# Performance work log

Hardware: AMD Instinct MI355X
Metric: run time of the kernel (lower is better)

## Reference

```python
import jax, jax.numpy as jnp
import numpy as np

B, S, T = 64, 48, 48
E, H = 256, 512
VIN, VOUT = 32000, 32000


def _gru_step(h, x, Wih, Whh, bih, bhh):
    # PyTorch GRU cell: gates ordered [r, z, n]
    gi = x @ Wih.T + bih            # [B, 3H]
    gh = h @ Whh.T + bhh            # [B, 3H]
    ir, iz, inn = jnp.split(gi, 3, axis=-1)
    hr, hz, hn = jnp.split(gh, 3, axis=-1)
    r = jax.nn.sigmoid(ir + hr)
    z = jax.nn.sigmoid(iz + hz)
    n = jnp.tanh(inn + r * hn)
    return (1.0 - z) * n + z * h


def setup_inputs() -> dict:
    key = jax.random.key(0)
    ks = jax.random.split(key, 24)
    scale = 0.05

    def w(k, shape):
        return jax.random.normal(k, shape, dtype=jnp.float32) * scale

    return {
        "source": jax.random.randint(ks[0], (B, S), 0, VIN),
        "target": jax.random.randint(ks[1], (B, T), 0, VOUT),
        "source_lengths": jax.random.randint(ks[2], (B,), 1, S + 1),
        "enc_emb": w(ks[3], (VIN, E)),
        "enc_Wih0": w(ks[4], (3 * H, E)),
        "enc_Whh0": w(ks[5], (3 * H, H)),
        "enc_bih0": w(ks[6], (3 * H,)),
        "enc_bhh0": w(ks[7], (3 * H,)),
        "enc_Wih1": w(ks[8], (3 * H, H)),
        "enc_Whh1": w(ks[9], (3 * H, H)),
        "enc_bih1": w(ks[10], (3 * H,)),
        "enc_bhh1": w(ks[11], (3 * H,)),
        "dec_emb": w(ks[12], (VOUT, E)),
        "dec_Wih0": w(ks[13], (3 * H, E)),
        "dec_Whh0": w(ks[14], (3 * H, H)),
        "dec_bih0": w(ks[15], (3 * H,)),
        "dec_bhh0": w(ks[16], (3 * H,)),
        "dec_Wih1": w(ks[17], (3 * H, H)),
        "dec_Whh1": w(ks[18], (3 * H, H)),
        "dec_bih1": w(ks[19], (3 * H,)),
        "dec_bhh1": w(ks[20], (3 * H,)),
        "fc_W": w(ks[21], (VOUT, H)),
        "fc_b": w(ks[22], (VOUT,)),
    }


def reference(source, target, source_lengths,
              enc_emb, enc_Wih0, enc_Whh0, enc_bih0, enc_bhh0,
              enc_Wih1, enc_Whh1, enc_bih1, enc_bhh1,
              dec_emb, dec_Wih0, dec_Whh0, dec_bih0, dec_bhh0,
              dec_Wih1, dec_Whh1, dec_bih1, dec_bhh1,
              fc_W, fc_b):
    # ---- Encoder: 2-layer GRU over packed (length-masked) source ----
    emb = enc_emb[source]                       # [B, S, E]
    xs = jnp.transpose(emb, (1, 0, 2))          # [S, B, E]
    ts = jnp.arange(S)
    h0 = jnp.zeros((B, H), emb.dtype)
    h1 = jnp.zeros((B, H), emb.dtype)

    def estep(carry, inp):
        c0, c1 = carry
        x_t, t = inp
        m = (t < source_lengths)[:, None]       # valid-step mask (packing semantics)
        n0 = _gru_step(c0, x_t, enc_Wih0, enc_Whh0, enc_bih0, enc_bhh0)
        n1 = _gru_step(c1, n0, enc_Wih1, enc_Whh1, enc_bih1, enc_bhh1)
        return (jnp.where(m, n0, c0), jnp.where(m, n1, c1)), None

    (h0, h1), _ = jax.lax.scan(estep, (h0, h1), (xs, ts))

    # ---- Decoder: teacher forcing (ratio=1.0) -> inputs are target[:, :-1] ----
    dec_in = dec_emb[target[:, :-1]]            # [B, T-1, E]
    dxs = jnp.transpose(dec_in, (1, 0, 2))      # [T-1, B, E]

    def dstep(carry, x_t):
        c0, c1 = carry
        n0 = _gru_step(c0, x_t, dec_Wih0, dec_Whh0, dec_bih0, dec_bhh0)
        n1 = _gru_step(c1, n0, dec_Wih1, dec_Whh1, dec_bih1, dec_bhh1)
        return (n0, n1), n1

    _, ys = jax.lax.scan(dstep, (h0, h1), dxs)  # [T-1, B, H]
    logits = jnp.einsum('tbh,vh->btv', ys, fc_W) + fc_b  # [B, T-1, V]
    # outputs[:, 0, :] stays zero as in the torch loop (starts at t=1)
    return jnp.concatenate([jnp.zeros((B, 1, VOUT), logits.dtype), logits], axis=1)
```

## Files before the change

kernel.cpp:

```cpp
#include <hip/hip_runtime.h>

#define B_    64
#define S_    48
#define T_    48
#define E_    256
#define H_    512
#define G_    1536
#define VOUT_ 32000
#define NBLK_ 48

typedef __attribute__((ext_vector_type(8))) short short8;
typedef __attribute__((ext_vector_type(4))) float f4;

__device__ inline unsigned short f2bf(float f) {
    unsigned u = __float_as_uint(f);
    u += 0x7fffu + ((u >> 16) & 1u);
    return (unsigned short)(u >> 16);
}
__device__ inline unsigned pack2(float a, float b) {
    return (unsigned)f2bf(a) | ((unsigned)f2bf(b) << 16);
}

__global__ void zero_f32(float* p, int n) {
    int i = blockIdx.x * 256 + threadIdx.x;
    if (i < n) p[i] = 0.f;
}

__global__ void zero_out_t0(float* out) {
    int v = blockIdx.x * 256 + threadIdx.x;
    int b = blockIdx.y;
    if (v < VOUT_) out[(size_t)b * T_ * VOUT_ + v] = 0.f;
}

__global__ void cvt_bf16(const float* __restrict__ s, unsigned short* __restrict__ d, int n4) {
    int i = blockIdx.x * 256 + threadIdx.x;
    if (i < n4) {
        float4 v = ((const float4*)s)[i];
        uint2 o;
        o.x = pack2(v.x, v.y);
        o.y = pack2(v.z, v.w);
        ((uint2*)d)[i] = o;
    }
}

__global__ __launch_bounds__(256)
void gemm64(const float* __restrict__ aF,
            const unsigned short* __restrict__ aB,
            const int* __restrict__ idx, int idx_stride,
            const unsigned short* __restrict__ Wb,
            const float* __restrict__ bias,
            float* __restrict__ outF,
            float* __restrict__ outR,
            int N, int K)
{
    __shared__ __align__(16) short As[64][40];
    __shared__ __align__(16) short Ws[64][40];
    const int tid  = threadIdx.x;
    const int m0   = blockIdx.x * 64;
    const int n0   = blockIdx.y * 64;
    const int row  = tid >> 2;
    const int col8 = (tid & 3) * 8;

    const float* apF = nullptr;
    const unsigned short* apB = nullptr;
    {
        int m = m0 + row;
        if (aF) {
            size_t r;
            if (idx) { int tt = m >> 6, b = m & 63; r = (size_t)idx[b * idx_stride + tt]; }
            else     { r = (size_t)m; }
            apF = aF + r * K + col8;
        } else {
            apB = aB + (size_t)m * K + col8;
        }
    }
    const unsigned short* wp = Wb + (size_t)(n0 + row) * K + col8;

    f4 acc[4];
    const f4 zz = {0.f, 0.f, 0.f, 0.f};
    acc[0] = zz; acc[1] = zz; acc[2] = zz; acc[3] = zz;

    const int wv   = tid >> 6;
    const int lane = tid & 63;
    const int quad = lane >> 4;
    const int l16  = lane & 15;

    for (int k0 = 0; k0 < K; k0 += 32) {
        uint4 av;
        if (apF) {
            float4 v0 = *(const float4*)(apF + k0);
            float4 v1 = *(const float4*)(apF + k0 + 4);
            av.x = pack2(v0.x, v0.y);
            av.y = pack2(v0.z, v0.w);
            av.z = pack2(v1.x, v1.y);
            av.w = pack2(v1.z, v1.w);
        } else {
            av = *(const uint4*)(apB + k0);
        }
        uint4 wvv = *(const uint4*)(wp + k0);
        *(uint4*)&As[row][col8] = av;
        *(uint4*)&Ws[row][col8] = wvv;
        __syncthreads();
        short8 afrag = *(const short8*)&As[wv * 16 + l16][quad * 8];
#pragma unroll
        for (int nt = 0; nt < 4; ++nt) {
            short8 bfrag = *(const short8*)&Ws[nt * 16 + l16][quad * 8];
            acc[nt] = __builtin_amdgcn_mfma_f32_16x16x32_bf16(afrag, bfrag, acc[nt], 0, 0, 0);
        }
        __syncthreads();
    }

#pragma unroll
    for (int nt = 0; nt < 4; ++nt) {
#pragma unroll
        for (int r = 0; r < 4; ++r) {
            int mm = m0 + wv * 16 + quad * 4 + r;
            int nn = n0 + nt * 16 + l16;
            float v = acc[nt][r];
            if (bias) v += bias[nn];
            if (outF) {
                outF[(size_t)mm * N + nn] = v;
            } else {
                int tt = mm >> 6, b = mm & 63;
                outR[((size_t)b * T_ + tt + 1) * VOUT_ + nn] = v;
            }
        }
    }
}

__device__ __forceinline__ void gsync(unsigned* bar, unsigned target) {
    __syncthreads();
    if (threadIdx.x == 0) {
        __threadfence();
        __hip_atomic_fetch_add(bar, 1u, __ATOMIC_RELAXED, __HIP_MEMORY_SCOPE_AGENT);
        while (__hip_atomic_load(bar, __ATOMIC_RELAXED, __HIP_MEMORY_SCOPE_AGENT) < target) {
            __builtin_amdgcn_s_sleep(1);
        }
        __threadfence();
    }
    __syncthreads();
}

__global__ __launch_bounds__(256, 1)
void scan_rnn(const unsigned short* __restrict__ Whh0,
              const unsigned short* __restrict__ Wih1,
              const unsigned short* __restrict__ Whh1,
              const float* __restrict__ gi,
              const float* __restrict__ bih1,
              const float* __restrict__ bhh0,
              const float* __restrict__ bhh1,
              float* __restrict__ h0F, float* __restrict__ h1F,
              unsigned short* __restrict__ h0b0, unsigned short* __restrict__ h0b1,
              unsigned short* __restrict__ h1b0, unsigned short* __restrict__ h1b1,
              unsigned short* __restrict__ n0b0, unsigned short* __restrict__ n0b1,
              unsigned short* __restrict__ ys,
              const int* __restrict__ lens,
              unsigned* __restrict__ bar, unsigned bar_base, int nsteps)
{
    __shared__ __align__(16) short8 Wl[96][64];

    const int tid   = threadIdx.x;
    const int bid   = blockIdx.x;
    const int wv    = tid >> 6;
    const int lane  = tid & 63;
    const int quad  = lane >> 4;
    const int l16   = lane & 15;
    const int quad8 = quad * 8;
    const int rowA  = wv * 16 + l16;
    const int mrow  = wv * 16 + quad * 4;
    const bool isL0 = bid < 16;
    const int j0    = isL0 ? bid * 32 : (bid - 16) * 16;
    const f4 zz = {0.f, 0.f, 0.f, 0.f};

#pragma unroll 4
    for (int i = 0; i < 24; ++i) {
        const int f = wv * 24 + i;
        const unsigned short* src;
        if (isL0) {
            int kiter = f / 6, rem = f % 6, g = rem >> 1, nt = rem & 1;
            src = Whh0 + (size_t)(g * H_ + j0 + nt * 16 + l16) * H_ + kiter * 32 + quad8;
        } else {
            int p = f / 48, rem = f % 48, kiter = rem / 3, g = rem % 3;
            const unsigned short* W = p ? Whh1 : Wih1;
            src = W + (size_t)(g * H_ + j0 + l16) * H_ + kiter * 32 + quad8;
        }
        Wl[f][lane] = *(const short8*)src;
    }
    __syncthreads();

    int lenm[4];
#pragma unroll
    for (int r = 0; r < 4; ++r) lenm[r] = lens ? lens[mrow + r] : 0x7fffffff;

    float b0r[2], b0z[2], b0n[2], h0r[2][4];
    float b1r = 0.f, b1z = 0.f, b1in = 0.f, b1hn = 0.f, h1r[4];
    if (isL0) {
#pragma unroll
        for (int nt = 0; nt < 2; ++nt) {
            const int j = j0 + nt * 16 + l16;
            b0r[nt] = bhh0[j]; b0z[nt] = bhh0[j + H_]; b0n[nt] = bhh0[j + 2 * H_];
#pragma unroll
            for (int r = 0; r < 4; ++r) h0r[nt][r] = h0F[(mrow + r) * H_ + j];
        }
    } else {
        const int j = j0 + l16;
        b1r  = bhh1[j] + bih1[j];
        b1z  = bhh1[j + H_] + bih1[j + H_];
        b1in = bih1[j + 2 * H_];
        b1hn = bhh1[j + 2 * H_];
#pragma unroll
        for (int r = 0; r < 4; ++r) h1r[r] = h1F[(mrow + r) * H_ + j];
    }

    for (int s = 0; s <= nsteps; ++s) {
        float gir[2][4], giz[2][4], gin[2][4];
        if (isL0 && s < nsteps) {
            const float* giT = gi + (size_t)s * (B_ * G_);
#pragma unroll
            for (int nt = 0; nt < 2; ++nt) {
                const int j = j0 + nt * 16 + l16;
#pragma unroll
                for (int r = 0; r < 4; ++r) {
                    const float* g = giT + (size_t)(mrow + r) * G_;
                    gir[nt][r] = g[j];
                    giz[nt][r] = g[j + H_];
                    gin[nt][r] = g[j + 2 * H_];
                }
            }
        }
        if (s) gsync(bar, bar_base + (unsigned)(NBLK_ * s));

        if (isL0) {
            const int t = s;
            if (t >= nsteps) continue;
            const int pi = t & 1;
            const unsigned short* Ab = pi ? h0b1 : h0b0;
            unsigned short* hob = pi ? h0b0 : h0b1;
            unsigned short* nob = pi ? n0b1 : n0b0;

            short8 av[16];
#pragma unroll
            for (int k = 0; k < 16; ++k)
                av[k] = *(const short8*)(Ab + (size_t)rowA * H_ + k * 32 + quad8);

            f4 acc[4][2];
#pragma unroll
            for (int a = 0; a < 4; ++a) { acc[a][0] = zz; acc[a][1] = zz; }
#pragma unroll
            for (int k = 0; k < 16; ++k) {
#pragma unroll
                for (int g = 0; g < 3; ++g) {
                    const int ai = (g == 2) ? 3 : g;
#pragma unroll
                    for (int nt = 0; nt < 2; ++nt) {
                        acc[ai][nt] = __builtin_amdgcn_mfma_f32_16x16x32_bf16(
                            av[k], Wl[k * 6 + g * 2 + nt][lane], acc[ai][nt], 0, 0, 0);
                    }
                }
            }

#pragma unroll
            for (int nt = 0; nt < 2; ++nt) {
                const int j = j0 + nt * 16 + l16;
#pragma unroll
                for (int r = 0; r < 4; ++r) {
                    const int m = mrow + r;
                    float pr = acc[0][nt][r] + b0r[nt] + gir[nt][r];
                    float pz = acc[1][nt][r] + b0z[nt] + giz[nt][r];
                    float hn = acc[3][nt][r] + b0n[nt];
                    float rg = 1.f / (1.f + expf(-pr));
                    float zg = 1.f / (1.f + expf(-pz));
                    float ng = tanhf(gin[nt][r] + rg * hn);
                    float hp = h0r[nt][r];
                    float hnew = (1.f - zg) * ng + zg * hp;
                    nob[m * H_ + j] = f2bf(hnew);
                    float hw = (t >= lenm[r]) ? hp : hnew;
                    h0r[nt][r] = hw;
                    hob[m * H_ + j] = f2bf(hw);
                    if (t == nsteps - 1) h0F[m * H_ + j] = hw;
                }
            }
        } else {
            const int t = s - 1;
            if (t < 0) continue;
            const int pi = t & 1;
            const unsigned short* xb = pi ? n0b1 : n0b0;
            const unsigned short* hb = pi ? h1b1 : h1b0;
            unsigned short* hob = pi ? h1b0 : h1b1;

            short8 av0[16], av1[16];
#pragma unroll
            for (int k = 0; k < 16; ++k) {
                av0[k] = *(const short8*)(xb + (size_t)rowA * H_ + k * 32 + quad8);
                av1[k] = *(const short8*)(hb + (size_t)rowA * H_ + k * 32 + quad8);
            }

            f4 acc[4];
#pragma unroll
            for (int a = 0; a < 4; ++a) acc[a] = zz;
#pragma unroll
            for (int k = 0; k < 16; ++k) {
#pragma unroll
                for (int g = 0; g < 3; ++g) {
                    const int ai = (g == 2) ? 2 : g;
                    acc[ai] = __builtin_amdgcn_mfma_f32_16x16x32_bf16(
                        av0[k], Wl[k * 3 + g][lane], acc[ai], 0, 0, 0);
                }
            }
#pragma unroll
            for (int k = 0; k < 16; ++k) {
#pragma unroll
                for (int g = 0; g < 3; ++g) {
                    const int ai = (g == 2) ? 3 : g;
                    acc[ai] = __builtin_amdgcn_mfma_f32_16x16x32_bf16(
                        av1[k], Wl[48 + k * 3 + g][lane], acc[ai], 0, 0, 0);
                }
            }

            const int j = j0 + l16;
#pragma unroll
            for (int r = 0; r < 4; ++r) {
                const int m = mrow + r;
                float pr  = acc[0][r] + b1r;
                float pz  = acc[1][r] + b1z;
                float inn = acc[2][r] + b1in;
                float hn  = acc[3][r] + b1hn;
                float rg = 1.f / (1.f + expf(-pr));
                float zg = 1.f / (1.f + expf(-pz));
                float ng = tanhf(inn + rg * hn);
                float hp = h1r[r];
                float hnew = (1.f - zg) * ng + zg * hp;
                if (ys) ys[((size_t)t * B_ + m) * H_ + j] = f2bf(hnew);
                float hw = (t >= lenm[r]) ? hp : hnew;
                h1r[r] = hw;
                hob[m * H_ + j] = f2bf(hw);
                if (t == nsteps - 1) h1F[m * H_ + j] = hw;
            }
        }
    }
}

static inline void cvt(const float* s, unsigned short* d, int n, hipStream_t st) {
    int n4 = n / 4;
    cvt_bf16<<<dim3((n4 + 255) / 256), 256, 0, st>>>(s, d, n4);
}

extern "C" void kernel_launch(void* const* d_in, const int* in_sizes, int n_in,
                              void* d_out, int out_size, void* d_ws, size_t ws_size,
                              hipStream_t stream)
{
    const int* source  = (const int*)d_in[0];
    const int* target  = (const int*)d_in[1];
    const int* src_len = (const int*)d_in[2];
    const float* enc_emb  = (const float*)d_in[3];
    const float* enc_Wih0 = (const float*)d_in[4];
    const float* enc_Whh0 = (const float*)d_in[5];
    const float* enc_bih0 = (const float*)d_in[6];
    const float* enc_bhh0 = (const float*)d_in[7];
    const float* enc_Wih1 = (const float*)d_in[8];
    const float* enc_Whh1 = (const float*)d_in[9];
    const float* enc_bih1 = (const float*)d_in[10];
    const float* enc_bhh1 = (const float*)d_in[11];
    const float* dec_emb  = (const float*)d_in[12];
    const float* dec_Wih0 = (const float*)d_in[13];
    const float* dec_Whh0 = (const float*)d_in[14];
    const float* dec_bih0 = (const float*)d_in[15];
    const float* dec_bhh0 = (const float*)d_in[16];
    const float* dec_Wih1 = (const float*)d_in[17];
    const float* dec_Whh1 = (const float*)d_in[18];
    const float* dec_bih1 = (const float*)d_in[19];
    const float* dec_bhh1 = (const float*)d_in[20];
    const float* fc_W     = (const float*)d_in[21];
    const float* fc_b     = (const float*)d_in[22];
    float* out = (float*)d_out;

    const size_t BH = (size_t)B_ * H_;

    char* w = (char*)d_ws;
    float* h0F = (float*)w;           w += BH * 4;
    float* h1F = (float*)w;           w += BH * 4;
    unsigned short* h0b0 = (unsigned short*)w; w += BH * 2;
    unsigned short* h1b0 = (unsigned short*)w; w += BH * 2;
    unsigned* bar = (unsigned*)w;     w += 256;
    unsigned short* h0b1 = (unsigned short*)w; w += BH * 2;
    unsigned short* h1b1 = (unsigned short*)w; w += BH * 2;
    unsigned short* n0b0 = (unsigned short*)w; w += BH * 2;
    unsigned short* n0b1 = (unsigned short*)w; w += BH * 2;
    float* gi_buf = (float*)w;                w += (size_t)S_ * B_ * G_ * 4;
    unsigned short* ys = (unsigned short*)w;  w += (size_t)(T_ - 1) * B_ * H_ * 2;
    unsigned short* eWih0b = (unsigned short*)w; w += (size_t)G_ * E_ * 2;
    unsigned short* dWih0b = (unsigned short*)w; w += (size_t)G_ * E_ * 2;
    unsigned short* eWih1b = (unsigned short*)w; w += (size_t)G_ * H_ * 2;
    unsigned short* eWhh0b = (unsigned short*)w; w += (size_t)G_ * H_ * 2;
    unsigned short* eWhh1b = (unsigned short*)w; w += (size_t)G_ * H_ * 2;
    unsigned short* dWih1b = (unsigned short*)w; w += (size_t)G_ * H_ * 2;
    unsigned short* dWhh0b = (unsigned short*)w; w += (size_t)G_ * H_ * 2;
    unsigned short* dWhh1b = (unsigned short*)w; w += (size_t)G_ * H_ * 2;
    unsigned short* fcWb   = (unsigned short*)w;

    cvt(enc_Wih0, eWih0b, G_ * E_, stream);
    cvt(dec_Wih0, dWih0b, G_ * E_, stream);
    cvt(enc_Wih1, eWih1b, G_ * H_, stream);
    cvt(enc_Whh0, eWhh0b, G_ * H_, stream);
    cvt(enc_Whh1, eWhh1b, G_ * H_, stream);
    cvt(dec_Wih1, dWih1b, G_ * H_, stream);
    cvt(dec_Whh0, dWhh0b, G_ * H_, stream);
    cvt(dec_Whh1, dWhh1b, G_ * H_, stream);
    cvt(fc_W,     fcWb,   VOUT_ * H_, stream);

    zero_f32<<<dim3((int)((3 * BH + 64 + 255) / 256)), 256, 0, stream>>>(
        (float*)d_ws, (int)(3 * BH) + 64);
    zero_out_t0<<<dim3((VOUT_ + 255) / 256, B_), 256, 0, stream>>>(out);

    gemm64<<<dim3(S_ * B_ / 64, G_ / 64), 256, 0, stream>>>(
        enc_emb, nullptr, source, S_, eWih0b, enc_bih0, gi_buf, nullptr, G_, E_);

    scan_rnn<<<NBLK_, 256, 0, stream>>>(
        eWhh0b, eWih1b, eWhh1b, gi_buf, enc_bih1, enc_bhh0, enc_bhh1,
        h0F, h1F, h0b0, h0b1, h1b0, h1b1, n0b0, n0b1,
        nullptr , src_len, bar, 0u, S_);

    gemm64<<<dim3((T_ - 1) * B_ / 64, G_ / 64), 256, 0, stream>>>(
        dec_emb, nullptr, target, T_, dWih0b, dec_bih0, gi_buf, nullptr, G_, E_);

    scan_rnn<<<NBLK_, 256, 0, stream>>>(
        dWhh0b, dWih1b, dWhh1b, gi_buf, dec_bih1, dec_bhh0, dec_bhh1,
        h0F, h1F, h0b0, h0b1, h1b0, h1b1, n0b0, n0b1,
        ys, nullptr , bar, (unsigned)(NBLK_ * S_), T_ - 1);

    gemm64<<<dim3((T_ - 1) * B_ / 64, VOUT_ / 64), 256, 0, stream>>>(
        nullptr, ys, nullptr, 0, fcWb, fc_b, nullptr, out, VOUT_, H_);
}
```

Measured before the change: 1.814 ms.

## Fuse encoder and decoder scans into one persistent kernel with split barriers

Merges the encoder and decoder recurrent scans into a single persistent launch, restaging decoder weights in LDS at the handoff step. The single global barrier is replaced by two per-layer counters with arrive-then-wait semantics, so layer-0 and layer-1 blocks wait only on what they depend on; a triple-buffered layer-0 output allows the extra slack. The weight conversions and zeroing are fused into one prep launch, gi buffers are split so both input GEMMs run before the scan, and fast sigmoid/tanh use exp plus hardware reciprocal. Risks include subtle ordering bugs from relaxed atomic loads and stores, and slightly lower activation accuracy.

```diff
diff --git a/kernel.cpp b/kernel.cpp
--- a/kernel.cpp
+++ b/kernel.cpp
@@ -8,6 +8,7 @@
 #define G_    1536
 #define VOUT_ 32000
 #define NBLK_ 48
+#define BH_   (B_ * H_)
 
 typedef __attribute__((ext_vector_type(8))) short short8;
 typedef __attribute__((ext_vector_type(4))) float f4;
@@ -21,26 +22,62 @@
     return (unsigned)f2bf(a) | ((unsigned)f2bf(b) << 16);
 }
 
-__global__ void zero_f32(float* p, int n) {
-    int i = blockIdx.x * 256 + threadIdx.x;
-    if (i < n) p[i] = 0.f;
+__device__ inline float sigf(float x) {
+    return __builtin_amdgcn_rcpf(1.f + __expf(-x));
+}
+__device__ inline float tanh_fast(float x) {
+    float e = __expf(-2.f * fabsf(x));
+    float r = (1.f - e) * __builtin_amdgcn_rcpf(1.f + e);
+    return copysignf(r, x);
+}
+
+__device__ inline short8 aload16(const unsigned short* p) {
+    union { unsigned long long u[2]; short8 s; } f;
+    const unsigned long long* q = (const unsigned long long*)p;
+    f.u[0] = __hip_atomic_load(q,     __ATOMIC_RELAXED, __HIP_MEMORY_SCOPE_AGENT);
+    f.u[1] = __hip_atomic_load(q + 1, __ATOMIC_RELAXED, __HIP_MEMORY_SCOPE_AGENT);
+    return f.s;
+}
+__device__ inline void ast16(unsigned short* p, unsigned short v) {
+    __hip_atomic_store(p, v, __ATOMIC_RELAXED, __HIP_MEMORY_SCOPE_AGENT);
+}
+
+#define NZ4_  32832
+#define ZBLK_ 129
+__global__ __launch_bounds__(256)
+void prep(const float* __restrict__ s0, const float* __restrict__ s1,
+          const float* __restrict__ s2, const float* __restrict__ s3,
+          const float* __restrict__ s4, const float* __restrict__ s5,
+          const float* __restrict__ s6, const float* __restrict__ s7,
+          const float* __restrict__ s8,
+          unsigned short* __restrict__ wt, unsigned* __restrict__ zbase)
+{
+    const int b = blockIdx.x, tid = threadIdx.x;
+    if (b < ZBLK_) {
+        int i = b * 256 + tid;
+        if (i < NZ4_) zbase[i] = 0u;
+        return;
+    }
+    int i = (b - ZBLK_) * 256 + tid;
+    const float* src; int off;
+    if      (i <   98304) { src = s0; off = 0;       }
+    else if (i <  196608) { src = s1; off =  98304;  }
+    else if (i <  393216) { src = s2; off = 196608;  }
+    else if (i <  589824) { src = s3; off = 393216;  }
+    else if (i <  786432) { src = s4; off = 589824;  }
+    else if (i <  983040) { src = s5; off = 786432;  }
+    else if (i < 1179648) { src = s6; off = 983040;  }
+    else if (i < 1376256) { src = s7; off = 1179648; }
+    else                  { src = s8; off = 1376256; }
+    float4 v = ((const float4*)src)[i - off];
+    uint2 o; o.x = pack2(v.x, v.y); o.y = pack2(v.z, v.w);
+    ((uint2*)wt)[i] = o;
 }
 
 __global__ void zero_out_t0(float* out) {
     int v = blockIdx.x * 256 + threadIdx.x;
     int b = blockIdx.y;
     if (v < VOUT_) out[(size_t)b * T_ * VOUT_ + v] = 0.f;
-}
-
-__global__ void cvt_bf16(const float* __restrict__ s, unsigned short* __restrict__ d, int n4) {
-    int i = blockIdx.x * 256 + threadIdx.x;
-    if (i < n4) {
-        float4 v = ((const float4*)s)[i];
-        uint2 o;
-        o.x = pack2(v.x, v.y);
-        o.y = pack2(v.z, v.w);
-        ((uint2*)d)[i] = o;
-    }
 }
 
 __global__ __launch_bounds__(256)
@@ -128,43 +165,29 @@
     }
 }
 
-__device__ __forceinline__ void gsync(unsigned* bar, unsigned target) {
-    __syncthreads();
-    if (threadIdx.x == 0) {
-        __threadfence();
-        __hip_atomic_fetch_add(bar, 1u, __ATOMIC_RELAXED, __HIP_MEMORY_SCOPE_AGENT);
-        while (__hip_atomic_load(bar, __ATOMIC_RELAXED, __HIP_MEMORY_SCOPE_AGENT) < target) {
-            __builtin_amdgcn_s_sleep(1);
-        }
-        __threadfence();
-    }
-    __syncthreads();
-}
-
 __global__ __launch_bounds__(256, 1)
-void scan_rnn(const unsigned short* __restrict__ Whh0,
-              const unsigned short* __restrict__ Wih1,
-              const unsigned short* __restrict__ Whh1,
-              const float* __restrict__ gi,
-              const float* __restrict__ bih1,
-              const float* __restrict__ bhh0,
-              const float* __restrict__ bhh1,
-              float* __restrict__ h0F, float* __restrict__ h1F,
+void scan_rnn(const unsigned short* __restrict__ eWhh0,
+              const unsigned short* __restrict__ eWih1,
+              const unsigned short* __restrict__ eWhh1,
+              const unsigned short* __restrict__ dWhh0,
+              const unsigned short* __restrict__ dWih1,
+              const unsigned short* __restrict__ dWhh1,
+              const float* __restrict__ giE, const float* __restrict__ giD,
+              const float* __restrict__ ebih1, const float* __restrict__ ebhh0,
+              const float* __restrict__ ebhh1,
+              const float* __restrict__ dbih1, const float* __restrict__ dbhh0,
+              const float* __restrict__ dbhh1,
               unsigned short* __restrict__ h0b0, unsigned short* __restrict__ h0b1,
               unsigned short* __restrict__ h1b0, unsigned short* __restrict__ h1b1,
-              unsigned short* __restrict__ n0b0, unsigned short* __restrict__ n0b1,
+              unsigned short* __restrict__ n0b,
               unsigned short* __restrict__ ys,
               const int* __restrict__ lens,
-              unsigned* __restrict__ bar, unsigned bar_base, int nsteps)
+              unsigned* __restrict__ barA, unsigned* __restrict__ barB)
 {
     __shared__ __align__(16) short8 Wl[96][64];
 
-    const int tid   = threadIdx.x;
-    const int bid   = blockIdx.x;
-    const int wv    = tid >> 6;
-    const int lane  = tid & 63;
-    const int quad  = lane >> 4;
-    const int l16   = lane & 15;
+    const int tid = threadIdx.x, bid = blockIdx.x;
+    const int wv = tid >> 6, lane = tid & 63, quad = lane >> 4, l16 = lane & 15;
     const int quad8 = quad * 8;
     const int rowA  = wv * 16 + l16;
     const int mrow  = wv * 16 + quad * 4;
@@ -172,50 +195,71 @@
     const int j0    = isL0 ? bid * 32 : (bid - 16) * 16;
     const f4 zz = {0.f, 0.f, 0.f, 0.f};
 
+    auto stage = [&](const unsigned short* W0, const unsigned short* W1) {
 #pragma unroll 4
-    for (int i = 0; i < 24; ++i) {
-        const int f = wv * 24 + i;
-        const unsigned short* src;
+        for (int i = 0; i < 24; ++i) {
+            const int f = wv * 24 + i;
+            const unsigned short* src;
+            if (isL0) {
+                int kiter = f / 6, rem = f % 6, g = rem >> 1, nt = rem & 1;
+                src = W0 + (size_t)(g * H_ + j0 + nt * 16 + l16) * H_ + kiter * 32 + quad8;
+            } else {
+                int p = f / 48, rem = f % 48, kiter = rem / 3, g = rem % 3;
+                const unsigned short* W = p ? W1 : W0;
+                src = W + (size_t)(g * H_ + j0 + l16) * H_ + kiter * 32 + quad8;
+            }
+            Wl[f][lane] = *(const short8*)src;
+        }
+    };
+
+    float b0r[2], b0z[2], b0n[2];
+    float b1r = 0.f, b1z = 0.f, b1in = 0.f, b1hn = 0.f;
+    auto hoist = [&](const float* bih1, const float* bhh0, const float* bhh1) {
         if (isL0) {
-            int kiter = f / 6, rem = f % 6, g = rem >> 1, nt = rem & 1;
-            src = Whh0 + (size_t)(g * H_ + j0 + nt * 16 + l16) * H_ + kiter * 32 + quad8;
+#pragma unroll
+            for (int nt = 0; nt < 2; ++nt) {
+                const int j = j0 + nt * 16 + l16;
+                b0r[nt] = bhh0[j]; b0z[nt] = bhh0[j + H_]; b0n[nt] = bhh0[j + 2 * H_];
+            }
         } else {
-            int p = f / 48, rem = f % 48, kiter = rem / 3, g = rem % 3;
-            const unsigned short* W = p ? Whh1 : Wih1;
-            src = W + (size_t)(g * H_ + j0 + l16) * H_ + kiter * 32 + quad8;
-        }
-        Wl[f][lane] = *(const short8*)src;
-    }
+            const int j = j0 + l16;
+            b1r  = bhh1[j] + bih1[j];
+            b1z  = bhh1[j + H_] + bih1[j + H_];
+            b1in = bih1[j + 2 * H_];
+            b1hn = bhh1[j + 2 * H_];
+        }
+    };
+
+    int lenm[4];
+#pragma unroll
+    for (int r = 0; r < 4; ++r) lenm[r] = lens[mrow + r];
+
+    float h0r[2][4] = {{0.f,0.f,0.f,0.f},{0.f,0.f,0.f,0.f}};
+    float h1r[4]    = {0.f,0.f,0.f,0.f};
+
+    if (isL0) stage(eWhh0, eWhh0); else stage(eWih1, eWhh1);
+    hoist(ebih1, ebhh0, ebhh1);
     __syncthreads();
 
-    int lenm[4];
-#pragma unroll
-    for (int r = 0; r < 4; ++r) lenm[r] = lens ? lens[mrow + r] : 0x7fffffff;
-
-    float b0r[2], b0z[2], b0n[2], h0r[2][4];
-    float b1r = 0.f, b1z = 0.f, b1in = 0.f, b1hn = 0.f, h1r[4];
-    if (isL0) {
-#pragma unroll
-        for (int nt = 0; nt < 2; ++nt) {
-            const int j = j0 + nt * 16 + l16;
-            b0r[nt] = bhh0[j]; b0z[nt] = bhh0[j + H_]; b0n[nt] = bhh0[j + 2 * H_];
-#pragma unroll
-            for (int r = 0; r < 4; ++r) h0r[nt][r] = h0F[(mrow + r) * H_ + j];
-        }
-    } else {
-        const int j = j0 + l16;
-        b1r  = bhh1[j] + bih1[j];
-        b1z  = bhh1[j + H_] + bih1[j + H_];
-        b1in = bih1[j + 2 * H_];
-        b1hn = bhh1[j + 2 * H_];
-#pragma unroll
-        for (int r = 0; r < 4; ++r) h1r[r] = h1F[(mrow + r) * H_ + j];
-    }
-
-    for (int s = 0; s <= nsteps; ++s) {
+    for (int s = 0; s < 97; ++s) {
+        const bool l0c = isL0 && (s < 48 || (s >= 49 && s < 96));
+        const bool l1c = (!isL0) && ((s >= 1 && s <= 48) || s >= 50);
+
+        if (s) {
+            asm volatile("s_waitcnt vmcnt(0)" ::: "memory");
+            __syncthreads();
+            if (tid == 0)
+                __hip_atomic_fetch_add(isL0 ? barA : barB, 1u,
+                                       __ATOMIC_RELAXED, __HIP_MEMORY_SCOPE_AGENT);
+        }
+
+        if (isL0 && s == 48) { stage(dWhh0, dWhh0); hoist(dbih1, dbhh0, dbhh1); }
+        if (!isL0 && s == 49) { stage(dWih1, dWhh1); hoist(dbih1, dbhh0, dbhh1); }
+
         float gir[2][4], giz[2][4], gin[2][4];
-        if (isL0 && s < nsteps) {
-            const float* giT = gi + (size_t)s * (B_ * G_);
+        if (l0c) {
+            const float* giT = (s < 48) ? giE + (size_t)s * (B_ * G_)
+                                        : giD + (size_t)(s - 49) * (B_ * G_);
 #pragma unroll
             for (int nt = 0; nt < 2; ++nt) {
                 const int j = j0 + nt * 16 + l16;
@@ -228,34 +272,48 @@
                 }
             }
         }
-        if (s) gsync(bar, bar_base + (unsigned)(NBLK_ * s));
+
+        if (s) {
+            if (tid == 0) {
+                const unsigned tA = 16u * (unsigned)s;
+                while (__hip_atomic_load(barA, __ATOMIC_RELAXED,
+                                         __HIP_MEMORY_SCOPE_AGENT) < tA)
+                    __builtin_amdgcn_s_sleep(1);
+                const unsigned tB = isL0 ? (s >= 2 ? 32u * (unsigned)(s - 1) : 0u)
+                                         : 32u * (unsigned)s;
+                while (__hip_atomic_load(barB, __ATOMIC_RELAXED,
+                                         __HIP_MEMORY_SCOPE_AGENT) < tB)
+                    __builtin_amdgcn_s_sleep(1);
+            }
+            __syncthreads();
+        }
 
         if (isL0) {
-            const int t = s;
-            if (t >= nsteps) continue;
-            const int pi = t & 1;
-            const unsigned short* Ab = pi ? h0b1 : h0b0;
-            unsigned short* hob = pi ? h0b0 : h0b1;
-            unsigned short* nob = pi ? n0b1 : n0b0;
+            if (!l0c) continue;
+            const bool enc = (s < 48);
+            const int t = enc ? s : s - 49;
+            const int a = enc ? s : s - 1;
+            const unsigned short* Ab = (a & 1) ? h0b1 : h0b0;
+            unsigned short* hob = (a & 1) ? h0b0 : h0b1;
+            unsigned short* nob = n0b + (size_t)(a % 3) * BH_;
 
             short8 av[16];
 #pragma unroll
             for (int k = 0; k < 16; ++k)
-                av[k] = *(const short8*)(Ab + (size_t)rowA * H_ + k * 32 + quad8);
+                av[k] = aload16(Ab + (size_t)rowA * H_ + k * 32 + quad8);
 
             f4 acc[4][2];
 #pragma unroll
-            for (int a = 0; a < 4; ++a) { acc[a][0] = zz; acc[a][1] = zz; }
+            for (int a2 = 0; a2 < 4; ++a2) { acc[a2][0] = zz; acc[a2][1] = zz; }
 #pragma unroll
             for (int k = 0; k < 16; ++k) {
 #pragma unroll
                 for (int g = 0; g < 3; ++g) {
                     const int ai = (g == 2) ? 3 : g;
 #pragma unroll
-                    for (int nt = 0; nt < 2; ++nt) {
+                    for (int nt = 0; nt < 2; ++nt)
                         acc[ai][nt] = __builtin_amdgcn_mfma_f32_16x16x32_bf16(
                             av[k], Wl[k * 6 + g * 2 + nt][lane], acc[ai][nt], 0, 0, 0);
-                    }
                 }
             }
 
@@ -268,36 +326,36 @@
                     float pr = acc[0][nt][r] + b0r[nt] + gir[nt][r];
                     float pz = acc[1][nt][r] + b0z[nt] + giz[nt][r];
                     float hn = acc[3][nt][r] + b0n[nt];
-                    float rg = 1.f / (1.f + expf(-pr));
-                    float zg = 1.f / (1.f + expf(-pz));
-                    float ng = tanhf(gin[nt][r] + rg * hn);
+                    float rg = sigf(pr);
+                    float zg = sigf(pz);
+                    float ng = tanh_fast(gin[nt][r] + rg * hn);
                     float hp = h0r[nt][r];
                     float hnew = (1.f - zg) * ng + zg * hp;
-                    nob[m * H_ + j] = f2bf(hnew);
-                    float hw = (t >= lenm[r]) ? hp : hnew;
+                    ast16(nob + m * H_ + j, f2bf(hnew));
+                    float hw = (enc && t >= lenm[r]) ? hp : hnew;
                     h0r[nt][r] = hw;
-                    hob[m * H_ + j] = f2bf(hw);
-                    if (t == nsteps - 1) h0F[m * H_ + j] = hw;
+                    ast16(hob + m * H_ + j, f2bf(hw));
                 }
             }
         } else {
-            const int t = s - 1;
-            if (t < 0) continue;
-            const int pi = t & 1;
-            const unsigned short* xb = pi ? n0b1 : n0b0;
-            const unsigned short* hb = pi ? h1b1 : h1b0;
-            unsigned short* hob = pi ? h1b0 : h1b1;
+            if (!l1c) continue;
+            const bool enc = (s <= 48);
+            const int t = enc ? s - 1 : s - 50;
+            const int a = enc ? s - 1 : s - 2;
+            const unsigned short* xb = n0b + (size_t)(a % 3) * BH_;
+            const unsigned short* hb = (a & 1) ? h1b1 : h1b0;
+            unsigned short* hob = (a & 1) ? h1b0 : h1b1;
 
             short8 av0[16], av1[16];
 #pragma unroll
             for (int k = 0; k < 16; ++k) {
-                av0[k] = *(const short8*)(xb + (size_t)rowA * H_ + k * 32 + quad8);
-                av1[k] = *(const short8*)(hb + (size_t)rowA * H_ + k * 32 + quad8);
+                av0[k] = aload16(xb + (size_t)rowA * H_ + k * 32 + quad8);
+                av1[k] = aload16(hb + (size_t)rowA * H_ + k * 32 + quad8);
             }
 
             f4 acc[4];
 #pragma unroll
-            for (int a = 0; a < 4; ++a) acc[a] = zz;
+            for (int a2 = 0; a2 < 4; ++a2) acc[a2] = zz;
 #pragma unroll
             for (int k = 0; k < 16; ++k) {
 #pragma unroll
@@ -325,24 +383,18 @@
                 float pz  = acc[1][r] + b1z;
                 float inn = acc[2][r] + b1in;
                 float hn  = acc[3][r] + b1hn;
-                float rg = 1.f / (1.f + expf(-pr));
-                float zg = 1.f / (1.f + expf(-pz));
-                float ng = tanhf(inn + rg * hn);
+                float rg = sigf(pr);
+                float zg = sigf(pz);
+                float ng = tanh_fast(inn + rg * hn);
                 float hp = h1r[r];
                 float hnew = (1.f - zg) * ng + zg * hp;
-                if (ys) ys[((size_t)t * B_ + m) * H_ + j] = f2bf(hnew);
-                float hw = (t >= lenm[r]) ? hp : hnew;
+                if (!enc) ys[((size_t)t * B_ + m) * H_ + j] = f2bf(hnew);
+                float hw = (enc && t >= lenm[r]) ? hp : hnew;
                 h1r[r] = hw;
-                hob[m * H_ + j] = f2bf(hw);
-                if (t == nsteps - 1) h1F[m * H_ + j] = hw;
+                ast16(hob + m * H_ + j, f2bf(hw));
             }
         }
     }
-}
-
-static inline void cvt(const float* s, unsigned short* d, int n, hipStream_t st) {
-    int n4 = n / 4;
-    cvt_bf16<<<dim3((n4 + 255) / 256), 256, 0, st>>>(s, d, n4);
 }
 
 extern "C" void kernel_launch(void* const* d_in, const int* in_sizes, int n_in,
@@ -374,60 +426,44 @@
     const float* fc_b     = (const float*)d_in[22];
     float* out = (float*)d_out;
 
-    const size_t BH = (size_t)B_ * H_;
-
     char* w = (char*)d_ws;
-    float* h0F = (float*)w;           w += BH * 4;
-    float* h1F = (float*)w;           w += BH * 4;
-    unsigned short* h0b0 = (unsigned short*)w; w += BH * 2;
-    unsigned short* h1b0 = (unsigned short*)w; w += BH * 2;
-    unsigned* bar = (unsigned*)w;     w += 256;
-    unsigned short* h0b1 = (unsigned short*)w; w += BH * 2;
-    unsigned short* h1b1 = (unsigned short*)w; w += BH * 2;
-    unsigned short* n0b0 = (unsigned short*)w; w += BH * 2;
-    unsigned short* n0b1 = (unsigned short*)w; w += BH * 2;
-    float* gi_buf = (float*)w;                w += (size_t)S_ * B_ * G_ * 4;
-    unsigned short* ys = (unsigned short*)w;  w += (size_t)(T_ - 1) * B_ * H_ * 2;
-    unsigned short* eWih0b = (unsigned short*)w; w += (size_t)G_ * E_ * 2;
-    unsigned short* dWih0b = (unsigned short*)w; w += (size_t)G_ * E_ * 2;
-    unsigned short* eWih1b = (unsigned short*)w; w += (size_t)G_ * H_ * 2;
-    unsigned short* eWhh0b = (unsigned short*)w; w += (size_t)G_ * H_ * 2;
-    unsigned short* eWhh1b = (unsigned short*)w; w += (size_t)G_ * H_ * 2;
-    unsigned short* dWih1b = (unsigned short*)w; w += (size_t)G_ * H_ * 2;
-    unsigned short* dWhh0b = (unsigned short*)w; w += (size_t)G_ * H_ * 2;
-    unsigned short* dWhh1b = (unsigned short*)w; w += (size_t)G_ * H_ * 2;
-    unsigned short* fcWb   = (unsigned short*)w;
-
-    cvt(enc_Wih0, eWih0b, G_ * E_, stream);
-    cvt(dec_Wih0, dWih0b, G_ * E_, stream);
-    cvt(enc_Wih1, eWih1b, G_ * H_, stream);
-    cvt(enc_Whh0, eWhh0b, G_ * H_, stream);
-    cvt(enc_Whh1, eWhh1b, G_ * H_, stream);
-    cvt(dec_Wih1, dWih1b, G_ * H_, stream);
-    cvt(dec_Whh0, dWhh0b, G_ * H_, stream);
-    cvt(dec_Whh1, dWhh1b, G_ * H_, stream);
-    cvt(fc_W,     fcWb,   VOUT_ * H_, stream);
-
-    zero_f32<<<dim3((int)((3 * BH + 64 + 255) / 256)), 256, 0, stream>>>(
-        (float*)d_ws, (int)(3 * BH) + 64);
+    unsigned short* h0b0v = (unsigned short*)w; w += (size_t)BH_ * 2;
+    unsigned short* h1b0v = (unsigned short*)w; w += (size_t)BH_ * 2;
+    unsigned* bar = (unsigned*)w;               w += 256;
+    unsigned short* h0b1v = (unsigned short*)w; w += (size_t)BH_ * 2;
+    unsigned short* h1b1v = (unsigned short*)w; w += (size_t)BH_ * 2;
+    unsigned short* n0bv  = (unsigned short*)w; w += (size_t)3 * BH_ * 2;
+    float* giE = (float*)w;  w += (size_t)S_ * B_ * G_ * 4;
+    float* giD = (float*)w;  w += (size_t)(T_ - 1) * B_ * G_ * 4;
+    unsigned short* ysv = (unsigned short*)w; w += (size_t)(T_ - 1) * B_ * H_ * 2;
+    unsigned short* wt  = (unsigned short*)w;
+    unsigned short* eWih0b = wt;
+    unsigned short* dWih0b = eWih0b + (size_t)G_ * E_;
+    unsigned short* eWih1b = dWih0b + (size_t)G_ * E_;
+    unsigned short* eWhh0b = eWih1b + (size_t)G_ * H_;
+    unsigned short* eWhh1b = eWhh0b + (size_t)G_ * H_;
+    unsigned short* dWih1b = eWhh1b + (size_t)G_ * H_;
+    unsigned short* dWhh0b = dWih1b + (size_t)G_ * H_;
+    unsigned short* dWhh1b = dWhh0b + (size_t)G_ * H_;
+    unsigned short* fcWb   = dWhh1b + (size_t)G_ * H_;
+
+    prep<<<dim3(ZBLK_ + 21376), 256, 0, stream>>>(
+        enc_Wih0, dec_Wih0, enc_Wih1, enc_Whh0, enc_Whh1,
+        dec_Wih1, dec_Whh0, dec_Whh1, fc_W, wt, (unsigned*)d_ws);
     zero_out_t0<<<dim3((VOUT_ + 255) / 256, B_), 256, 0, stream>>>(out);
 
     gemm64<<<dim3(S_ * B_ / 64, G_ / 64), 256, 0, stream>>>(
-        enc_emb, nullptr, source, S_, eWih0b, enc_bih0, gi_buf, nullptr, G_, E_);
+        enc_emb, nullptr, source, S_, eWih0b, enc_bih0, giE, nullptr, G_, E_);
+    gemm64<<<dim3((T_ - 1) * B_ / 64, G_ / 64), 256, 0, stream>>>(
+        dec_emb, nullptr, target, T_, dWih0b, dec_bih0, giD, nullptr, G_, E_);
 
     scan_rnn<<<NBLK_, 256, 0, stream>>>(
-        eWhh0b, eWih1b, eWhh1b, gi_buf, enc_bih1, enc_bhh0, enc_bhh1,
-        h0F, h1F, h0b0, h0b1, h1b0, h1b1, n0b0, n0b1,
-        nullptr , src_len, bar, 0u, S_);
-
-    gemm64<<<dim3((T_ - 1) * B_ / 64, G_ / 64), 256, 0, stream>>>(
-        dec_emb, nullptr, target, T_, dWih0b, dec_bih0, gi_buf, nullptr, G_, E_);
-
-    scan_rnn<<<NBLK_, 256, 0, stream>>>(
-        dWhh0b, dWih1b, dWhh1b, gi_buf, dec_bih1, dec_bhh0, dec_bhh1,
-        h0F, h1F, h0b0, h0b1, h1b0, h1b1, n0b0, n0b1,
-        ys, nullptr , bar, (unsigned)(NBLK_ * S_), T_ - 1);
+        eWhh0b, eWih1b, eWhh1b, dWhh0b, dWih1b, dWhh1b,
+        giE, giD,
+        enc_bih1, enc_bhh0, enc_bhh1, dec_bih1, dec_bhh0, dec_bhh1,
+        h0b0v, h0b1v, h1b0v, h1b1v, n0bv, ysv, src_len,
+        bar, bar + 32);
 
     gemm64<<<dim3((T_ - 1) * B_ / 64, VOUT_ / 64), 256, 0, stream>>>(
-        nullptr, ys, nullptr, 0, fcWb, fc_b, nullptr, out, VOUT_, H_);
-}
+        nullptr, ysv, nullptr, 0, fcWb, fc_b, nullptr, out, VOUT_, H_);
+}
```

Result: slower. 1.965 ms (+8.3%).
